# Performance work log

Measured on AMD Instinct MI355X. Metric: run time of the kernel, lower is better.

## Reference

```python
import jax, jax.numpy as jnp
import numpy as np

N, E, G = 150000, 600000, 5000
NI, EI, GF, H, C = 16, 8, 32, 64, 40


def setup_inputs() -> dict:
    key = jax.random.key(0)
    ks = jax.random.split(key, 20)
    s = lambda fan: 1.0 / np.sqrt(fan)
    return {
        "x": jax.random.normal(ks[0], (N, NI), jnp.float32),
        "edge_index": jax.random.randint(ks[1], (2, E), 0, N),
        "edge_attr": jax.random.normal(ks[2], (E, EI), jnp.float32),
        "batch": jnp.sort(jax.random.randint(ks[3], (N,), 0, G)),
        "pocket_features": jax.random.normal(ks[4], (G, GF), jnp.float32),
        # edge MLP: Linear(EI,H) -> ReLU -> Linear(H, H*NI)
        "W_e1": jax.random.normal(ks[5], (EI, H), jnp.float32) * s(EI),
        "b_e1": jnp.zeros((H,), jnp.float32),
        "W_e2": jax.random.normal(ks[6], (H, H * NI), jnp.float32) * s(H),
        "b_e2": jnp.zeros((H * NI,), jnp.float32),
        # NNConv root weight + bias
        "root": jax.random.normal(ks[7], (NI, H), jnp.float32) * s(NI),
        "conv_bias": jnp.zeros((H,), jnp.float32),
        # GlobalAttention gate Linear(H,1)
        "Wg": jax.random.normal(ks[8], (H, 1), jnp.float32) * s(H),
        "bg": jnp.zeros((1,), jnp.float32),
        # fc1: input is concat [h_node(H), global_ctx(H), pocket(GF)]
        "W_fc1": jax.random.normal(ks[9], (2 * H + GF, H), jnp.float32) * s(2 * H + GF),
        "b_fc1": jnp.zeros((H,), jnp.float32),
        "W_np": jax.random.normal(ks[10], (H, C), jnp.float32) * s(H),
        "b_np": jnp.zeros((C,), jnp.float32),
        "W_sp": jax.random.normal(ks[11], (H, 1), jnp.float32) * s(H),
        "b_sp": jnp.zeros((1,), jnp.float32),
    }


def reference(x, edge_index, edge_attr, batch, pocket_features,
              W_e1, b_e1, W_e2, b_e2, root, conv_bias, Wg, bg,
              W_fc1, b_fc1, W_np, b_np, W_sp, b_sp):
    n, ni = x.shape
    h = root.shape[1]
    g = pocket_features.shape[0]
    src, dst = edge_index[0], edge_index[1]

    # NNConv: edge MLP -> per-edge weight matrix [E, NI, H]
    eh = jax.nn.relu(edge_attr @ W_e1 + b_e1)
    We = (eh @ W_e2 + b_e2).reshape(-1, ni, h)
    msg = jnp.einsum('ei,eih->eh', x[src], We)          # per-edge matmul
    agg = jax.ops.segment_sum(msg, dst, num_segments=n)
    cnt = jax.ops.segment_sum(jnp.ones(msg.shape[0], x.dtype), dst, num_segments=n)
    agg = agg / jnp.maximum(cnt, 1.0)[:, None]          # aggr='mean'
    h_node = jax.nn.relu(agg + x @ root + conv_bias)    # [N, H]

    # GlobalAttention pooling: scatter-softmax over nodes per graph
    gate = (h_node @ Wg + bg).squeeze(-1)               # [N]
    m = jax.ops.segment_max(gate, batch, num_segments=g)
    e = jnp.exp(gate - m[batch])
    denom = jax.ops.segment_sum(e, batch, num_segments=g)
    attn = e / denom[batch]
    gctx = jax.ops.segment_sum(attn[:, None] * h_node, batch, num_segments=g)
    gc = gctx[batch]                                    # broadcast back [N, H]

    feat = jnp.concatenate([h_node, gc, pocket_features[batch]], axis=1)
    f = jax.nn.relu(feat @ W_fc1 + b_fc1)
    node_pred = jax.nn.log_softmax(f @ W_np + b_np, axis=-1)
    stop = jax.nn.sigmoid((gc @ W_sp + b_sp).squeeze(-1))
    return node_pred, stop
```

## Files before the change

### kernel.cpp

```cpp
#include <hip/hip_runtime.h>
#include <hip/hip_bf16.h>
#include <math.h>

#define NN 150000
#define EE 600000
#define GG 5000
#define NI 16
#define EI 8
#define GFD 32
#define HH 64
#define CC 40

#define W2SZ (68 * 1024)
#define EHS 72
#define FPAD 68
#define NBLK ((NN + 1023) / 1024)

typedef __attribute__((ext_vector_type(8))) short short8v;
typedef __attribute__((ext_vector_type(8))) unsigned short ushort8v;
typedef __attribute__((ext_vector_type(16))) float f32x16;
typedef __attribute__((ext_vector_type(2))) float f32x2;

__device__ __forceinline__ unsigned short f2bf(float f) {
    __hip_bfloat16 h = __float2bfloat16(f);
    return __builtin_bit_cast(unsigned short, h);
}
__device__ __forceinline__ float bf2f(unsigned short u) {
    return __uint_as_float(((unsigned)u) << 16);
}
__device__ __forceinline__ unsigned cvtpk(float lo, float hi) {
    unsigned r;
    asm("v_cvt_pk_bf16_f32 %0, %1, %2" : "=v"(r) : "v"(lo), "v"(hi));
    return r;
}
__device__ __forceinline__ f32x2 pkmul(f32x2 a, f32x2 b) {
    f32x2 p;
    asm("v_pk_mul_f32 %0, %1, %2" : "=v"(p) : "v"(a), "v"(b));
    return p;
}
__device__ __forceinline__ short8v zfrag(float eh, const f32x2 (&xs2)[4]) {
    f32x2 ehp; ehp[0] = eh; ehp[1] = eh;
    union { short8v v; unsigned u[4]; } A;
    #pragma unroll
    for (int q = 0; q < 4; ++q) {
        f32x2 p = pkmul(ehp, xs2[q]);
        A.u[q] = cvtpk(p[0], p[1]);
    }
    return A.v;
}
__device__ __forceinline__ short8v xfrag(const f32x2 (&xs2)[4]) {
    union { short8v v; unsigned u[4]; } A;
    #pragma unroll
    for (int q = 0; q < 4; ++q)
        A.u[q] = cvtpk(xs2[q][0], xs2[q][1]);
    return A.v;
}

__global__ void k0_prep(const float* __restrict__ W_e2, const float* __restrict__ b_e2,
                        const float* __restrict__ W_fc1, const float* __restrict__ W_np,
                        const float* __restrict__ W_e1,
                        unsigned short* __restrict__ W2c,
                        unsigned short* __restrict__ W1aT,
                        unsigned short* __restrict__ W_npT,
                        unsigned short* __restrict__ W1e,
                        int* __restrict__ cursor, int* __restrict__ gcur)
{
    int idx = blockIdx.x * 256 + threadIdx.x;
    if (idx < W2SZ) {
        int c = idx >> 10, rem = idx & 1023;
        int r = rem >> 4, kk = rem & 15;
        float v = 0.f;
        if (c < 64)       v = W_e2[c * 1024 + kk * 64 + r];
        else if (c == 64) v = b_e2[kk * 64 + r];
        W2c[idx] = f2bf(v);
    } else if (idx < W2SZ + 4096) {
        int i = idx - W2SZ;
        int h = i >> 6, k = i & 63;
        W1aT[i] = f2bf(W_fc1[k * 64 + h]);
    } else if (idx < W2SZ + 8192) {
        int i = idx - W2SZ - 4096;
        int c = i >> 6, h = i & 63;
        W_npT[i] = f2bf(c < CC ? W_np[h * CC + c] : 0.f);
    } else if (idx < W2SZ + 8704) {
        int i = idx - W2SZ - 8192;
        int col = i >> 3, q = i & 7;
        W1e[i] = f2bf(W_e1[q * 64 + col]);
    } else if (idx < W2SZ + 8704 + NN) {
        cursor[idx - W2SZ - 8704] = 0;
    } else if (idx == W2SZ + 8704 + NN) {
        gcur[0] = 0;
    }
}

__global__ void kE_local(const int* __restrict__ ei, int* __restrict__ cursor,
                         int* __restrict__ rank)
{
    int e = blockIdx.x * 256 + threadIdx.x;
    if (e < EE) rank[e] = atomicAdd(&cursor[ei[EE + e]], 1);
}

__global__ void kB_scan(const int* __restrict__ cnt, int* __restrict__ base,
                        int* __restrict__ gcur)
{
    __shared__ int sS[256];
    __shared__ int sOff;
    int b = blockIdx.x, t = threadIdx.x;
    int i0 = b * 1024 + t * 4;
    int v0 = (i0 + 0 < NN) ? cnt[i0 + 0] : 0;
    int v1 = (i0 + 1 < NN) ? cnt[i0 + 1] : 0;
    int v2 = (i0 + 2 < NN) ? cnt[i0 + 2] : 0;
    int v3 = (i0 + 3 < NN) ? cnt[i0 + 3] : 0;
    int tot = v0 + v1 + v2 + v3;
    sS[t] = tot;
    __syncthreads();
    int acc = tot;
    for (int off = 1; off < 256; off <<= 1) {
        int xv = (t >= off) ? sS[t - off] : 0;
        __syncthreads();
        acc += xv;
        sS[t] = acc;
        __syncthreads();
    }
    if (t == 255) sOff = atomicAdd(gcur, acc);
    __syncthreads();
    int run = acc - tot + sOff;
    if (i0 + 0 < NN) base[i0 + 0] = run; run += v0;
    if (i0 + 1 < NN) base[i0 + 1] = run; run += v1;
    if (i0 + 2 < NN) base[i0 + 2] = run; run += v2;
    if (i0 + 3 < NN) base[i0 + 3] = run;
}

template<bool TWOPHASE>
__global__ __launch_bounds__(256, 4) void k1_mfma(
    const float* __restrict__ x, const int* __restrict__ ei,
    const float* __restrict__ ea,
    const unsigned short* __restrict__ W1e, const float* __restrict__ b_e1,
    const unsigned short* __restrict__ W2c,
    const int* __restrict__ rank, const int* __restrict__ base,
    unsigned* __restrict__ msg16, float* __restrict__ agg)
{
    __shared__ unsigned short sEHT2[256][EHS];
    __shared__ int sIdx[256];

    const int t = threadIdx.x;
    const long long eb = (long long)blockIdx.x * 256;

    const int lane = t & 63;
    const int w = t >> 6;
    const int mr = lane & 31;
    const int half = lane >> 5;
    const int mb = w * 64;

    {
        long long ge = eb + t;
        if (ge < EE) {
            int d = ei[EE + ge];
            sIdx[t] = TWOPHASE ? (base[d] + rank[ge]) : d;
        } else {
            sIdx[t] = -1;
        }
    }

    {
        short8v bW0, bW1;
        if (half == 0) {
            bW0 = *(const short8v*)(W1e + (size_t)mr * 8);
            bW1 = *(const short8v*)(W1e + (size_t)(32 + mr) * 8);
        } else {
            #pragma unroll
            for (int q = 0; q < 8; ++q) { bW0[q] = 0; bW1[q] = 0; }
        }
        float bias0 = b_e1[mr];
        float bias1 = b_e1[32 + mr];
        #pragma unroll
        for (int m = 0; m < 2; ++m) {
            long long ge = eb + mb + m * 32 + mr;
            short8v a;
            if (half == 0 && ge < EE) {
                const float4* eap = (const float4*)(ea + ge * EI);
                float4 u0 = eap[0], u1 = eap[1];
                union { short8v v; unsigned u[4]; } A;
                A.u[0] = cvtpk(u0.x, u0.y); A.u[1] = cvtpk(u0.z, u0.w);
                A.u[2] = cvtpk(u1.x, u1.y); A.u[3] = cvtpk(u1.z, u1.w);
                a = A.v;
            } else {
                #pragma unroll
                for (int q = 0; q < 8; ++q) a[q] = 0;
            }
            #pragma unroll
            for (int n = 0; n < 2; ++n) {
                f32x16 c_;
                #pragma unroll
                for (int r = 0; r < 16; ++r) c_[r] = 0.f;
                c_ = __builtin_amdgcn_mfma_f32_32x32x16_bf16(a, n ? bW1 : bW0, c_, 0, 0, 0);
                int kcol = n * 32 + mr;
                float bias = n ? bias1 : bias0;
                #pragma unroll
                for (int r = 0; r < 16; ++r) {
                    int row = (r & 3) + 8 * (r >> 2) + 4 * half;
                    sEHT2[mb + m * 32 + row][kcol] = f2bf(fmaxf(c_[r] + bias, 0.f));
                }
            }
        }
    }

    f32x2 xs0[4], xs1[4];
    {
        long long g0 = eb + mb + mr;
        long long g1 = g0 + 32;
        if (g0 < EE) {
            int s0 = ei[g0];
            const float4* xp = (const float4*)(x + (size_t)s0 * NI + half * 8);
            float4 u0 = xp[0], u1 = xp[1];
            xs0[0][0]=u0.x; xs0[0][1]=u0.y; xs0[1][0]=u0.z; xs0[1][1]=u0.w;
            xs0[2][0]=u1.x; xs0[2][1]=u1.y; xs0[3][0]=u1.z; xs0[3][1]=u1.w;
        } else {
            #pragma unroll
            for (int q = 0; q < 4; ++q) { xs0[q][0] = 0.f; xs0[q][1] = 0.f; }
        }
        if (g1 < EE) {
            int s1 = ei[g1];
            const float4* xp = (const float4*)(x + (size_t)s1 * NI + half * 8);
            float4 u0 = xp[0], u1 = xp[1];
            xs1[0][0]=u0.x; xs1[0][1]=u0.y; xs1[1][0]=u0.z; xs1[1][1]=u0.w;
            xs1[2][0]=u1.x; xs1[2][1]=u1.y; xs1[3][0]=u1.z; xs1[3][1]=u1.w;
        } else {
            #pragma unroll
            for (int q = 0; q < 4; ++q) { xs1[q][0] = 0.f; xs1[q][1] = 0.f; }
        }
    }
    __syncthreads();

    f32x16 acc00, acc01, acc10, acc11;
    #pragma unroll
    for (int r = 0; r < 16; ++r) { acc00[r] = 0.f; acc01[r] = 0.f; acc10[r] = 0.f; acc11[r] = 0.f; }

    const unsigned short* Bq0 = W2c + mr * 16 + half * 8;
    const unsigned short* Bq1 = Bq0 + 512;

    short8v bA0 = *(const short8v*)(Bq0);
    short8v bA1 = *(const short8v*)(Bq1);
    short8v bB0 = *(const short8v*)(Bq0 + 1024);
    short8v bB1 = *(const short8v*)(Bq1 + 1024);

    const unsigned short* ehp0 = &sEHT2[mb + mr][0];
    const unsigned short* ehp1 = ehp0 + 32 * EHS;

    ushort8v eh0 = *(const ushort8v*)(ehp0);
    ushort8v eh1 = *(const ushort8v*)(ehp1);

    #pragma unroll 1
    for (int cb = 0; cb < 64; cb += 8) {
        ushort8v nx0 = *(const ushort8v*)(ehp0 + cb + 8);
        ushort8v nx1 = *(const ushort8v*)(ehp1 + cb + 8);
        #pragma unroll
        for (int j = 0; j < 8; j += 2) {
            int c = cb + j;
            {
                short8v p0 = *(const short8v*)(Bq0 + (c + 2) * 1024);
                short8v p1 = *(const short8v*)(Bq1 + (c + 2) * 1024);
                short8v a0 = zfrag(bf2f(eh0[j]), xs0);
                short8v a1 = zfrag(bf2f(eh1[j]), xs1);
                __builtin_amdgcn_s_setprio(1);
                acc00 = __builtin_amdgcn_mfma_f32_32x32x16_bf16(a0, bA0, acc00, 0, 0, 0);
                acc01 = __builtin_amdgcn_mfma_f32_32x32x16_bf16(a0, bA1, acc01, 0, 0, 0);
                acc10 = __builtin_amdgcn_mfma_f32_32x32x16_bf16(a1, bA0, acc10, 0, 0, 0);
                acc11 = __builtin_amdgcn_mfma_f32_32x32x16_bf16(a1, bA1, acc11, 0, 0, 0);
                __builtin_amdgcn_s_setprio(0);
                bA0 = p0; bA1 = p1;
            }
            {
                short8v p0 = *(const short8v*)(Bq0 + (c + 3) * 1024);
                short8v p1 = *(const short8v*)(Bq1 + (c + 3) * 1024);
                short8v a0 = zfrag(bf2f(eh0[j + 1]), xs0);
                short8v a1 = zfrag(bf2f(eh1[j + 1]), xs1);
                __builtin_amdgcn_s_setprio(1);
                acc00 = __builtin_amdgcn_mfma_f32_32x32x16_bf16(a0, bB0, acc00, 0, 0, 0);
                acc01 = __builtin_amdgcn_mfma_f32_32x32x16_bf16(a0, bB1, acc01, 0, 0, 0);
                acc10 = __builtin_amdgcn_mfma_f32_32x32x16_bf16(a1, bB0, acc10, 0, 0, 0);
                acc11 = __builtin_amdgcn_mfma_f32_32x32x16_bf16(a1, bB1, acc11, 0, 0, 0);
                __builtin_amdgcn_s_setprio(0);
                bB0 = p0; bB1 = p1;
            }
        }
        eh0 = nx0; eh1 = nx1;
    }
    {
        short8v a0 = xfrag(xs0);
        short8v a1 = xfrag(xs1);
        __builtin_amdgcn_s_setprio(1);
        acc00 = __builtin_amdgcn_mfma_f32_32x32x16_bf16(a0, bA0, acc00, 0, 0, 0);
        acc01 = __builtin_amdgcn_mfma_f32_32x32x16_bf16(a0, bA1, acc01, 0, 0, 0);
        acc10 = __builtin_amdgcn_mfma_f32_32x32x16_bf16(a1, bA0, acc10, 0, 0, 0);
        acc11 = __builtin_amdgcn_mfma_f32_32x32x16_bf16(a1, bA1, acc11, 0, 0, 0);
        __builtin_amdgcn_s_setprio(0);
    }

    #pragma unroll
    for (int r = 0; r < 16; ++r) {
        int row = (r & 3) + 8 * (r >> 2) + 4 * half;
        int i0 = sIdx[mb + row];
        int i1 = sIdx[mb + 32 + row];
        if (TWOPHASE) {
            if (i0 >= 0) msg16[(size_t)i0 * 32 + mr] = cvtpk(acc00[r], acc01[r]);
            if (i1 >= 0) msg16[(size_t)i1 * 32 + mr] = cvtpk(acc10[r], acc11[r]);
        } else {
            if (i0 >= 0) {
                atomicAdd(&agg[(size_t)i0 * 64 + mr],      acc00[r]);
                atomicAdd(&agg[(size_t)i0 * 64 + 32 + mr], acc01[r]);
            }
            if (i1 >= 0) {
                atomicAdd(&agg[(size_t)i1 * 64 + mr],      acc10[r]);
                atomicAdd(&agg[(size_t)i1 * 64 + 32 + mr], acc11[r]);
            }
        }
    }
}

__global__ __launch_bounds__(256) void k2_red(
    const unsigned* __restrict__ msg16, const int* __restrict__ base,
    const int* __restrict__ deg,
    const float* __restrict__ x, const float* __restrict__ root,
    const float* __restrict__ conv_bias,
    unsigned short* __restrict__ hn16,
    const float* __restrict__ Wg, const float* __restrict__ bg,
    float* __restrict__ gate)
{
    __shared__ float sroot[16][64];
    int t = threadIdx.x;
    #pragma unroll
    for (int q = 0; q < 4; ++q) {
        int i = q * 256 + t;
        sroot[i >> 6][i & 63] = root[i];
    }
    __syncthreads();

    int n = blockIdx.x * 4 + (t >> 6);
    int l = t & 63;
    int mr = l & 31, so = l >> 5;
    int s = base[n];
    int e = s + deg[n];

    float alo = 0.f, ahi = 0.f;
    int sl = s + so;
    for (; sl + 2 < e; sl += 4) {
        unsigned u0 = msg16[(size_t)sl * 32 + mr];
        unsigned u1 = msg16[(size_t)(sl + 2) * 32 + mr];
        alo += __uint_as_float(u0 << 16) + __uint_as_float(u1 << 16);
        ahi += __uint_as_float(u0 & 0xFFFF0000u) + __uint_as_float(u1 & 0xFFFF0000u);
    }
    if (sl < e) {
        unsigned u = msg16[(size_t)sl * 32 + mr];
        alo += __uint_as_float(u << 16);
        ahi += __uint_as_float(u & 0xFFFF0000u);
    }
    alo += __shfl_xor(alo, 32);
    ahi += __shfl_xor(ahi, 32);
    float acc = (l < 32) ? alo : ahi;

    float inv = 1.0f / fmaxf((float)(e - s), 1.0f);
    float v = acc * inv + conv_bias[l];
    float xv = (l < 16) ? x[(size_t)n * NI + l] : 0.f;
    #pragma unroll
    for (int i = 0; i < 16; ++i)
        v = fmaf(__shfl(xv, i), sroot[i][l], v);
    v = fmaxf(v, 0.f);
    hn16[(size_t)n * 64 + l] = f2bf(v);

    float gv = v * Wg[l];
    #pragma unroll
    for (int off = 32; off; off >>= 1) gv += __shfl_xor(gv, off);
    if (l == 0) gate[n] = gv + bg[0];
}

__global__ __launch_bounds__(256) void k2_node(
    const float* __restrict__ agg, const int* __restrict__ deg,
    const float* __restrict__ x, const float* __restrict__ root,
    const float* __restrict__ conv_bias,
    unsigned short* __restrict__ hn16,
    const float* __restrict__ Wg, const float* __restrict__ bg,
    float* __restrict__ gate)
{
    int t = threadIdx.x;
    int n = blockIdx.x * 4 + (t >> 6);
    int h = t & 63;
    float inv = 1.0f / fmaxf((float)deg[n], 1.0f);
    float v = agg[(size_t)n * 64 + h] * inv + conv_bias[h];
    const float* xp = x + (size_t)n * NI;
    #pragma unroll
    for (int i = 0; i < NI; ++i) v += xp[i] * root[i * 64 + h];
    v = fmaxf(v, 0.f);
    hn16[(size_t)n * 64 + h] = f2bf(v);
    float gv = v * Wg[h];
    #pragma unroll
    for (int off = 32; off; off >>= 1) gv += __shfl_xor(gv, off);
    if (h == 0) gate[n] = gv + bg[0];
}

__device__ __forceinline__ int lbound(const int* __restrict__ b, int v) {
    int lo = 0, hi = NN;
    while (lo < hi) { int mid = (lo + hi) >> 1; if (b[mid] < v) lo = mid + 1; else hi = mid; }
    return lo;
}

__global__ __launch_bounds__(64) void k3_pool(
    const float* __restrict__ gate, const int* __restrict__ batch,
    const unsigned short* __restrict__ hn16, const float* __restrict__ pocket,
    const float* __restrict__ W_fc1, const float* __restrict__ b_fc1,
    const float* __restrict__ W_sp, const float* __restrict__ b_sp,
    float* __restrict__ pg, float* __restrict__ sg)
{
    int g = blockIdx.x;
    int lane = threadIdx.x;
    int s = lbound(batch, g);
    int e = lbound(batch, g + 1);

    float gcv = 0.f;
    if (e > s) {
        float m = -INFINITY;
        for (int n = s + lane; n < e; n += 64) m = fmaxf(m, gate[n]);
        #pragma unroll
        for (int off = 32; off; off >>= 1) m = fmaxf(m, __shfl_xor(m, off));
        float acc = 0.f, den = 0.f;
        int n = s;
        for (; n + 2 <= e; n += 2) {
            float e0 = expf(gate[n] - m);
            float e1 = expf(gate[n + 1] - m);
            float h0 = bf2f(hn16[(size_t)n * 64 + lane]);
            float h1 = bf2f(hn16[(size_t)(n + 1) * 64 + lane]);
            den += e0 + e1;
            acc = fmaf(e0, h0, acc);
            acc = fmaf(e1, h1, acc);
        }
        if (n < e) {
            float ev = expf(gate[n] - m);
            den += ev;
            acc = fmaf(ev, bf2f(hn16[(size_t)n * 64 + lane]), acc);
        }
        gcv = acc / den;
    }

    float sv = gcv * W_sp[lane];
    #pragma unroll
    for (int off = 32; off; off >>= 1) sv += __shfl_xor(sv, off);
    if (lane == 0) sg[g] = 1.f / (1.f + expf(-(sv + b_sp[0])));

    float pk = (lane < GFD) ? pocket[(size_t)g * GFD + lane] : 0.f;
    float pgv = b_fc1[lane];
    #pragma unroll 8
    for (int kk = 0; kk < 64; ++kk)
        pgv = fmaf(__shfl(gcv, kk), W_fc1[(64 + kk) * 64 + lane], pgv);
    #pragma unroll 8
    for (int kk = 0; kk < 32; ++kk)
        pgv = fmaf(__shfl(pk, kk), W_fc1[(128 + kk) * 64 + lane], pgv);
    pg[(size_t)g * 64 + lane] = pgv;
}

__global__ __launch_bounds__(256, 4) void k4_mfma(
    const unsigned short* __restrict__ hn16, const int* __restrict__ batch,
    const float* __restrict__ pg, const float* __restrict__ sg,
    const unsigned short* __restrict__ W1aT, const unsigned short* __restrict__ W_npT,
    const float* __restrict__ b_np,
    float* __restrict__ out_np, float* __restrict__ out_stop)
{
    __shared__ __align__(16) float sF[4][32][FPAD];
    __shared__ int sB[128];

    const int t = threadIdx.x;
    const int wv = t >> 6, lane = t & 63;
    const int mr = lane & 31, half = lane >> 5;
    const int nb = blockIdx.x * 128;

    if (t < 128) {
        int n = nb + t;
        sB[t] = (n < NN) ? batch[n] : 0;
    }

    const int node = nb + wv * 32 + mr;

    f32x16 acc0, acc1;
    #pragma unroll
    for (int r = 0; r < 16; ++r) { acc0[r] = 0.f; acc1[r] = 0.f; }

    #pragma unroll
    for (int c = 0; c < 4; ++c) {
        short8v a;
        if (node < NN) {
            a = *(const short8v*)(hn16 + (size_t)node * 64 + c * 16 + half * 8);
        } else {
            #pragma unroll
            for (int q = 0; q < 8; ++q) a[q] = 0;
        }
        short8v b0 = *(const short8v*)(W1aT + (size_t)mr * 64        + c * 16 + half * 8);
        short8v b1 = *(const short8v*)(W1aT + (size_t)(mr + 32) * 64 + c * 16 + half * 8);
        acc0 = __builtin_amdgcn_mfma_f32_32x32x16_bf16(a, b0, acc0, 0, 0, 0);
        acc1 = __builtin_amdgcn_mfma_f32_32x32x16_bf16(a, b1, acc1, 0, 0, 0);
    }
    __syncthreads();

    #pragma unroll
    for (int r = 0; r < 16; ++r) {
        int row = (r & 3) + 8 * (r >> 2) + 4 * half;
        int g = sB[wv * 32 + row];
        float p0 = pg[(size_t)g * 64 + mr];
        float p1 = pg[(size_t)g * 64 + 32 + mr];
        sF[wv][row][mr]      = fmaxf(acc0[r] + p0, 0.f);
        sF[wv][row][32 + mr] = fmaxf(acc1[r] + p1, 0.f);
    }

    f32x16 acc2, acc3;
    #pragma unroll
    for (int r = 0; r < 16; ++r) { acc2[r] = 0.f; acc3[r] = 0.f; }

    #pragma unroll
    for (int c = 0; c < 4; ++c) {
        const float* fp = &sF[wv][mr][c * 16 + half * 8];
        float4 u0 = *(const float4*)(fp);
        float4 u1 = *(const float4*)(fp + 4);
        union { short8v v; unsigned u[4]; } A;
        A.u[0] = cvtpk(u0.x, u0.y); A.u[1] = cvtpk(u0.z, u0.w);
        A.u[2] = cvtpk(u1.x, u1.y); A.u[3] = cvtpk(u1.z, u1.w);
        short8v a = A.v;
        short8v b0 = *(const short8v*)(W_npT + (size_t)mr * 64        + c * 16 + half * 8);
        short8v b1 = *(const short8v*)(W_npT + (size_t)(mr + 32) * 64 + c * 16 + half * 8);
        acc2 = __builtin_amdgcn_mfma_f32_32x32x16_bf16(a, b0, acc2, 0, 0, 0);
        acc3 = __builtin_amdgcn_mfma_f32_32x32x16_bf16(a, b1, acc3, 0, 0, 0);
    }

    float bn1 = b_np[mr];
    float bn2 = (mr < 8) ? b_np[32 + mr] : 0.f;

    #pragma unroll
    for (int r = 0; r < 16; ++r) {
        int row = (r & 3) + 8 * (r >> 2) + 4 * half;
        int n = nb + wv * 32 + row;
        float v1 = acc2[r] + bn1;
        float v2 = acc3[r] + bn2;
        float m = (mr < 8) ? fmaxf(v1, v2) : v1;
        #pragma unroll
        for (int off = 16; off; off >>= 1) m = fmaxf(m, __shfl_xor(m, off));
        float s = expf(v1 - m) + ((mr < 8) ? expf(v2 - m) : 0.f);
        #pragma unroll
        for (int off = 16; off; off >>= 1) s += __shfl_xor(s, off);
        float ls = m + logf(s);
        if (n < NN) {
            out_np[(size_t)n * CC + mr] = v1 - ls;
            if (mr < 8) out_np[(size_t)n * CC + 32 + mr] = v2 - ls;
            if (mr == 0) out_stop[n] = sg[sB[wv * 32 + row]];
        }
    }
}

extern "C" void kernel_launch(void* const* d_in, const int* in_sizes, int n_in,
                              void* d_out, int out_size, void* d_ws, size_t ws_size,
                              hipStream_t stream)
{
    (void)in_sizes; (void)n_in; (void)out_size;
    const float* x        = (const float*)d_in[0];
    const int*   ei       = (const int*)d_in[1];
    const float* ea       = (const float*)d_in[2];
    const int*   batch    = (const int*)d_in[3];
    const float* pocket   = (const float*)d_in[4];
    const float* W_e1     = (const float*)d_in[5];
    const float* b_e1     = (const float*)d_in[6];
    const float* W_e2     = (const float*)d_in[7];
    const float* b_e2     = (const float*)d_in[8];
    const float* root     = (const float*)d_in[9];
    const float* conv_b   = (const float*)d_in[10];
    const float* Wg       = (const float*)d_in[11];
    const float* bg       = (const float*)d_in[12];
    const float* W_fc1    = (const float*)d_in[13];
    const float* b_fc1    = (const float*)d_in[14];
    const float* W_np     = (const float*)d_in[15];
    const float* b_np     = (const float*)d_in[16];
    const float* W_sp     = (const float*)d_in[17];
    const float* b_sp     = (const float*)d_in[18];

    char* wsb = (char*)d_ws;
    float* agg    = (float*)wsb;
    int*   base   = (int*)(agg + (size_t)NN * 64);
    int*   gcur   = base + NN;
    int*   cursor = gcur + 4;
    int*   rank   = cursor + NN;
    float* gate   = (float*)(rank + EE);
    float* pg     = gate + NN;
    float* sg     = pg + (size_t)GG * 64;
    unsigned short* hn16  = (unsigned short*)(sg + GG);
    unsigned short* W2c   = hn16 + (size_t)NN * 64;
    unsigned short* W1aT  = W2c + W2SZ;
    unsigned short* W_npT = W1aT + 4096;
    unsigned short* W1e   = W_npT + 4096;
    size_t head = (size_t)((char*)(W1e + 512) - wsb);
    size_t msg_off = (head + 255) & ~(size_t)255;
    unsigned* msg16 = (unsigned*)(wsb + msg_off);
    size_t need = msg_off + (size_t)EE * 32 * sizeof(unsigned);
    const bool twophase = (ws_size >= need);

    k0_prep<<<(W2SZ + 8705 + NN + 255) / 256, 256, 0, stream>>>(
        W_e2, b_e2, W_fc1, W_np, W_e1, W2c, W1aT, W_npT, W1e, cursor, gcur);

    kE_local<<<(EE + 255) / 256, 256, 0, stream>>>(ei, cursor, rank);
    kB_scan<<<NBLK, 256, 0, stream>>>(cursor, base, gcur);

    if (twophase) {
        k1_mfma<true><<<(EE + 255) / 256, 256, 0, stream>>>(
            x, ei, ea, W1e, b_e1, W2c, rank, base, msg16, agg);
        k2_red<<<NN / 4, 256, 0, stream>>>(msg16, base, cursor, x, root, conv_b,
                                           hn16, Wg, bg, gate);
    } else {
        hipMemsetAsync(agg, 0, (size_t)NN * 64 * sizeof(float), stream);
        k1_mfma<false><<<(EE + 255) / 256, 256, 0, stream>>>(
            x, ei, ea, W1e, b_e1, W2c, rank, base, msg16, agg);
        k2_node<<<NN / 4, 256, 0, stream>>>(agg, cursor, x, root, conv_b,
                                            hn16, Wg, bg, gate);
    }

    k3_pool<<<GG, 64, 0, stream>>>(gate, batch, hn16, pocket, W_fc1, b_fc1, W_sp, b_sp, pg, sg);

    float* out_np   = (float*)d_out;
    float* out_stop = out_np + (size_t)NN * CC;
    k4_mfma<<<(NN + 127) / 128, 256, 0, stream>>>(hn16, batch, pg, sg, W1aT, W_npT, b_np,
                                                  out_np, out_stop);
}
```

Before: 262.0 us.

## Transpose edge-hidden LDS tile with XOR swizzle; precompute graph bounds

The per-edge hidden activations in shared memory move from an edge-major padded layout to a channel-major [65][256] layout with an XOR swizzle. The store side now writes packed bf16 pairs, and the MFMA loop reads one scalar per channel, which is meant to reduce LDS bank conflicts and pack conversions. A new small kernel computes per-graph node start offsets from the sorted batch array, replacing two binary searches per graph in the pooling kernel. The cost is an extra kernel launch, plus scalar LDS reads per step in place of vector loads.

```diff
diff --git a/kernel.cpp b/kernel.cpp
--- a/kernel.cpp
+++ b/kernel.cpp
@@ -12,12 +12,10 @@
 #define CC 40
 
 #define W2SZ (68 * 1024)
-#define EHS 72
 #define FPAD 68
 #define NBLK ((NN + 1023) / 1024)
 
 typedef __attribute__((ext_vector_type(8))) short short8v;
-typedef __attribute__((ext_vector_type(8))) unsigned short ushort8v;
 typedef __attribute__((ext_vector_type(16))) float f32x16;
 typedef __attribute__((ext_vector_type(2))) float f32x2;
 
@@ -130,6 +128,40 @@
     if (i0 + 3 < NN) base[i0 + 3] = run;
 }
 
+__global__ void kG_bounds(const int* __restrict__ batch, int* __restrict__ gs)
+{
+    int n = blockIdx.x * 256 + threadIdx.x;
+    if (n >= NN) return;
+    int b1 = batch[n];
+    int b0 = (n == 0) ? -1 : batch[n - 1];
+    for (int g = b0 + 1; g <= b1; ++g) gs[g] = n;
+    if (n == NN - 1)
+        for (int g = b1 + 1; g <= GG; ++g) gs[g] = NN;
+}
+
+__device__ __forceinline__ void mfma_step(
+    const unsigned short (&sEHT)[65][256], int c, int pf,
+    const unsigned short* __restrict__ Bq0, const unsigned short* __restrict__ Bq1,
+    int mb, int mr, const f32x2 (&xs0)[4], const f32x2 (&xs1)[4],
+    short8v& curb0, short8v& curb1,
+    f32x16& acc00, f32x16& acc01, f32x16& acc10, f32x16& acc11)
+{
+    short8v n0 = *(const short8v*)(Bq0 + pf * 1024);
+    short8v n1 = *(const short8v*)(Bq1 + pf * 1024);
+    int cc = (c & 31) << 1;
+    float eh0 = bf2f(sEHT[c][(mb + mr) ^ cc]);
+    float eh1 = bf2f(sEHT[c][(mb + 32 + mr) ^ cc]);
+    short8v a0 = zfrag(eh0, xs0);
+    short8v a1 = zfrag(eh1, xs1);
+    __builtin_amdgcn_s_setprio(1);
+    acc00 = __builtin_amdgcn_mfma_f32_32x32x16_bf16(a0, curb0, acc00, 0, 0, 0);
+    acc01 = __builtin_amdgcn_mfma_f32_32x32x16_bf16(a0, curb1, acc01, 0, 0, 0);
+    acc10 = __builtin_amdgcn_mfma_f32_32x32x16_bf16(a1, curb0, acc10, 0, 0, 0);
+    acc11 = __builtin_amdgcn_mfma_f32_32x32x16_bf16(a1, curb1, acc11, 0, 0, 0);
+    __builtin_amdgcn_s_setprio(0);
+    curb0 = n0; curb1 = n1;
+}
+
 template<bool TWOPHASE>
 __global__ __launch_bounds__(256, 4) void k1_mfma(
     const float* __restrict__ x, const int* __restrict__ ei,
@@ -139,7 +171,7 @@
     const int* __restrict__ rank, const int* __restrict__ base,
     unsigned* __restrict__ msg16, float* __restrict__ agg)
 {
-    __shared__ unsigned short sEHT2[256][EHS];
+    __shared__ unsigned short sEHT[65][256];
     __shared__ int sIdx[256];
 
     const int t = threadIdx.x;
@@ -159,6 +191,7 @@
         } else {
             sIdx[t] = -1;
         }
+        sEHT[64][t] = (unsigned short)0x3F80;
     }
 
     {
@@ -196,9 +229,12 @@
                 int kcol = n * 32 + mr;
                 float bias = n ? bias1 : bias0;
                 #pragma unroll
-                for (int r = 0; r < 16; ++r) {
+                for (int r = 0; r < 16; r += 2) {
                     int row = (r & 3) + 8 * (r >> 2) + 4 * half;
-                    sEHT2[mb + m * 32 + row][kcol] = f2bf(fmaxf(c_[r] + bias, 0.f));
+                    int e0 = mb + m * 32 + row;
+                    float v0 = fmaxf(c_[r]     + bias, 0.f);
+                    float v1 = fmaxf(c_[r + 1] + bias, 0.f);
+                    *(unsigned*)&sEHT[kcol][e0 ^ (mr << 1)] = cvtpk(v0, v1);
                 }
             }
         }
@@ -243,47 +279,10 @@
     short8v bB0 = *(const short8v*)(Bq0 + 1024);
     short8v bB1 = *(const short8v*)(Bq1 + 1024);
 
-    const unsigned short* ehp0 = &sEHT2[mb + mr][0];
-    const unsigned short* ehp1 = ehp0 + 32 * EHS;
-
-    ushort8v eh0 = *(const ushort8v*)(ehp0);
-    ushort8v eh1 = *(const ushort8v*)(ehp1);
-
-    #pragma unroll 1
-    for (int cb = 0; cb < 64; cb += 8) {
-        ushort8v nx0 = *(const ushort8v*)(ehp0 + cb + 8);
-        ushort8v nx1 = *(const ushort8v*)(ehp1 + cb + 8);
-        #pragma unroll
-        for (int j = 0; j < 8; j += 2) {
-            int c = cb + j;
-            {
-                short8v p0 = *(const short8v*)(Bq0 + (c + 2) * 1024);
-                short8v p1 = *(const short8v*)(Bq1 + (c + 2) * 1024);
-                short8v a0 = zfrag(bf2f(eh0[j]), xs0);
-                short8v a1 = zfrag(bf2f(eh1[j]), xs1);
-                __builtin_amdgcn_s_setprio(1);
-                acc00 = __builtin_amdgcn_mfma_f32_32x32x16_bf16(a0, bA0, acc00, 0, 0, 0);
-                acc01 = __builtin_amdgcn_mfma_f32_32x32x16_bf16(a0, bA1, acc01, 0, 0, 0);
-                acc10 = __builtin_amdgcn_mfma_f32_32x32x16_bf16(a1, bA0, acc10, 0, 0, 0);
-                acc11 = __builtin_amdgcn_mfma_f32_32x32x16_bf16(a1, bA1, acc11, 0, 0, 0);
-                __builtin_amdgcn_s_setprio(0);
-                bA0 = p0; bA1 = p1;
-            }
-            {
-                short8v p0 = *(const short8v*)(Bq0 + (c + 3) * 1024);
-                short8v p1 = *(const short8v*)(Bq1 + (c + 3) * 1024);
-                short8v a0 = zfrag(bf2f(eh0[j + 1]), xs0);
-                short8v a1 = zfrag(bf2f(eh1[j + 1]), xs1);
-                __builtin_amdgcn_s_setprio(1);
-                acc00 = __builtin_amdgcn_mfma_f32_32x32x16_bf16(a0, bB0, acc00, 0, 0, 0);
-                acc01 = __builtin_amdgcn_mfma_f32_32x32x16_bf16(a0, bB1, acc01, 0, 0, 0);
-                acc10 = __builtin_amdgcn_mfma_f32_32x32x16_bf16(a1, bB0, acc10, 0, 0, 0);
-                acc11 = __builtin_amdgcn_mfma_f32_32x32x16_bf16(a1, bB1, acc11, 0, 0, 0);
-                __builtin_amdgcn_s_setprio(0);
-                bB0 = p0; bB1 = p1;
-            }
-        }
-        eh0 = nx0; eh1 = nx1;
+    #pragma unroll 2
+    for (int c = 0; c < 64; c += 2) {
+        mfma_step(sEHT, c,     c + 2, Bq0, Bq1, mb, mr, xs0, xs1, bA0, bA1, acc00, acc01, acc10, acc11);
+        mfma_step(sEHT, c + 1, c + 3, Bq0, Bq1, mb, mr, xs0, xs1, bB0, bB1, acc00, acc01, acc10, acc11);
     }
     {
         short8v a0 = xfrag(xs0);
@@ -397,14 +396,8 @@
     if (h == 0) gate[n] = gv + bg[0];
 }
 
-__device__ __forceinline__ int lbound(const int* __restrict__ b, int v) {
-    int lo = 0, hi = NN;
-    while (lo < hi) { int mid = (lo + hi) >> 1; if (b[mid] < v) lo = mid + 1; else hi = mid; }
-    return lo;
-}
-
 __global__ __launch_bounds__(64) void k3_pool(
-    const float* __restrict__ gate, const int* __restrict__ batch,
+    const float* __restrict__ gate, const int* __restrict__ gs,
     const unsigned short* __restrict__ hn16, const float* __restrict__ pocket,
     const float* __restrict__ W_fc1, const float* __restrict__ b_fc1,
     const float* __restrict__ W_sp, const float* __restrict__ b_sp,
@@ -412,8 +405,8 @@
 {
     int g = blockIdx.x;
     int lane = threadIdx.x;
-    int s = lbound(batch, g);
-    int e = lbound(batch, g + 1);
+    int s = gs[g];
+    int e = gs[g + 1];
 
     float gcv = 0.f;
     if (e > s) {
@@ -582,7 +575,8 @@
     int*   gcur   = base + NN;
     int*   cursor = gcur + 4;
     int*   rank   = cursor + NN;
-    float* gate   = (float*)(rank + EE);
+    int*   gs     = rank + EE;
+    float* gate   = (float*)(gs + GG + 4);
     float* pg     = gate + NN;
     float* sg     = pg + (size_t)GG * 64;
     unsigned short* hn16  = (unsigned short*)(sg + GG);
@@ -601,6 +595,7 @@
 
     kE_local<<<(EE + 255) / 256, 256, 0, stream>>>(ei, cursor, rank);
     kB_scan<<<NBLK, 256, 0, stream>>>(cursor, base, gcur);
+    kG_bounds<<<(NN + 255) / 256, 256, 0, stream>>>(batch, gs);
 
     if (twophase) {
         k1_mfma<true><<<(EE + 255) / 256, 256, 0, stream>>>(
@@ -615,7 +610,7 @@
                                             hn16, Wg, bg, gate);
     }
 
-    k3_pool<<<GG, 64, 0, stream>>>(gate, batch, hn16, pocket, W_fc1, b_fc1, W_sp, b_sp, pg, sg);
+    k3_pool<<<GG, 64, 0, stream>>>(gate, gs, hn16, pocket, W_fc1, b_fc1, W_sp, b_sp, pg, sg);
 
     float* out_np   = (float*)d_out;
     float* out_stop = out_np + (size_t)NN * CC;
```

New measurement: 248.6 us. 1.05x faster.
